# Optimization experiments

Hardware: AMD Instinct MI355X
Metric: run time of the kernel (lower is better)

## Reference

```python
import jax, jax.numpy as jnp
import numpy as np

TOP_K = 2
NUM_EXPERTS = 8

def setup_inputs() -> dict:
    key = jax.random.key(0)
    k_x, k_r, k_g, k_u, k_d = jax.random.split(key, 5)
    B, L, D, H, E = 1, 2048, 1024, 2048, NUM_EXPERTS
    scale = 0.02  # keep router logits / activations in a sane range
    return {
        "x": jax.random.normal(k_x, (B, L, D), dtype=jnp.float32),
        "router_w": jax.random.normal(k_r, (D, E), dtype=jnp.float32) * scale,
        "gate_w": jax.random.normal(k_g, (E, D, H), dtype=jnp.float32) * scale,
        "up_w": jax.random.normal(k_u, (E, D, H), dtype=jnp.float32) * scale,
        "down_w": jax.random.normal(k_d, (E, H, D), dtype=jnp.float32) * scale,
    }

def reference(x, router_w, gate_w, up_w, down_w):
    # x: (B, L, D)
    B, L, D = x.shape
    T = B * L
    E = router_w.shape[1]
    xf = x.reshape(T, D)

    # --- router: top-k softmax over selected logits (Mixtral-style) ---
    logits = xf @ router_w                      # (T, E)
    top_vals, top_idx = jax.lax.top_k(logits, TOP_K)  # (T, K)
    top_w = jax.nn.softmax(top_vals, axis=-1)   # (T, K)

    # combine weights scattered to dense (T, E); zeros for unrouted experts
    combine = jnp.zeros((T, E), dtype=x.dtype).at[
        jnp.arange(T)[:, None], top_idx
    ].add(top_w)

    # --- experts: SwiGLU, computed per expert, zero-weight tokens masked by combine ---
    gate = jnp.einsum('td,edh->eth', xf, gate_w)   # (E, T, H)
    up = jnp.einsum('td,edh->eth', xf, up_w)       # (E, T, H)
    hidden = jax.nn.silu(gate) * up                # (E, T, H)
    expert_out = jnp.einsum('eth,ehd->etd', hidden, down_w)  # (E, T, D)

    # --- weighted combine (equivalent to scatter_add over sorted assignments) ---
    y = jnp.einsum('etd,te->td', expert_out, combine)  # (T, D)
    return y.reshape(B, L, D)
```

## Files before the change

### kernel.cpp

```cpp
#include <hip/hip_runtime.h>
#include <hip/hip_bf16.h>
#include <stdint.h>

#define T_TOK 2048
#define DIM   1024
#define HDIM  2048
#define NE    8
#define ROWS_PAD 4224
#define TSLOTS 40

typedef __attribute__((ext_vector_type(8))) short bf16x8;
typedef __attribute__((ext_vector_type(4))) float f32x4;

__device__ __forceinline__ unsigned short f2bf(float f) {
    union { float f; unsigned int u; } v; v.f = f;
    unsigned int r = v.u + 0x7FFF + ((v.u >> 16) & 1);
    return (unsigned short)(r >> 16);
}

__device__ __forceinline__ void gload16(const void* g, void* l) {
    __builtin_amdgcn_global_load_lds(
        (const __attribute__((address_space(1))) void*)g,
        (__attribute__((address_space(3))) void*)l, 16, 0, 0);
}

__global__ void transpose_cvt(const float* __restrict__ in, unsigned short* __restrict__ out,
                              int R, int C) {
    __shared__ float tile[32][33];
    int b = blockIdx.z;
    int bx = blockIdx.x, by = blockIdx.y;
    int tx = threadIdx.x & 31, ty = threadIdx.x >> 5;
    const float* ip = in + (size_t)b * R * C;
    unsigned short* op = out + (size_t)b * R * C;
#pragma unroll
    for (int i = 0; i < 4; ++i) {
        int r = by * 32 + ty + i * 8;
        tile[ty + i * 8][tx] = ip[(size_t)r * C + bx * 32 + tx];
    }
    __syncthreads();
#pragma unroll
    for (int i = 0; i < 2; ++i) {
        int oc = i * 16 + (threadIdx.x >> 4);
        int orw2 = (threadIdx.x & 15) * 2;
        ushort2 v;
        v.x = f2bf(tile[orw2][oc]);
        v.y = f2bf(tile[orw2 + 1][oc]);
        *(ushort2*)&op[(size_t)(bx * 32 + oc) * R + by * 32 + orw2] = v;
    }
}

__global__ void router_kernel(const float* __restrict__ x, const float* __restrict__ rw,
                              int* __restrict__ counts, int* __restrict__ top_idx,
                              float* __restrict__ top_w) {
    int wid = (blockIdx.x * blockDim.x + threadIdx.x) >> 6;
    int lane = threadIdx.x & 63;
    if (wid >= T_TOK) return;
    float acc[NE];
#pragma unroll
    for (int e = 0; e < NE; ++e) acc[e] = 0.f;
    const float* xr = x + (size_t)wid * DIM;
    for (int i = lane; i < DIM; i += 64) {
        float xv = xr[i];
        const float* wr = rw + (size_t)i * NE;
#pragma unroll
        for (int e = 0; e < NE; ++e) acc[e] += xv * wr[e];
    }
#pragma unroll
    for (int off = 32; off; off >>= 1) {
#pragma unroll
        for (int e = 0; e < NE; ++e) acc[e] += __shfl_xor(acc[e], off, 64);
    }
    if (lane == 0) {
        float v0 = -1e30f, v1 = -1e30f; int i0 = 0, i1 = 0;
#pragma unroll
        for (int e = 0; e < NE; ++e) {
            float v = acc[e];
            if (v > v0) { v1 = v0; i1 = i0; v0 = v; i0 = e; }
            else if (v > v1) { v1 = v; i1 = e; }
        }
        float e1 = __expf(v1 - v0);
        float s = 1.f + e1;
        top_idx[wid * 2]     = i0;
        top_idx[wid * 2 + 1] = i1;
        top_w[wid * 2]     = 1.f / s;
        top_w[wid * 2 + 1] = e1 / s;
        atomicAdd(&counts[i0], 1);
        atomicAdd(&counts[i1], 1);
    }
}

__global__ void scan_kernel(const int* __restrict__ counts, int* __restrict__ offsets,
                            int* __restrict__ cursors,
                            int* __restrict__ tl_e, int* __restrict__ tl_m) {
    if (threadIdx.x == 0) {
        int run = 0;
        for (int e = 0; e < NE; ++e) { offsets[e] = run; cursors[e] = run; run += counts[e]; }
        int n = 0;
        for (int e = 0; e < NE; ++e) {
            int mt = (counts[e] + 127) >> 7;
            for (int m = 0; m < mt && n < 64; ++m) { tl_e[n] = e; tl_m[n] = m; ++n; }
        }
        for (; n < 64; ++n) tl_e[n] = -1;
    }
}

__global__ void gather_kernel(const float* __restrict__ x, const int* __restrict__ top_idx,
                              const float* __restrict__ top_w, int* __restrict__ cursors,
                              int* __restrict__ row_tok, float* __restrict__ row_w,
                              unsigned short* __restrict__ Abuf) {
    int t = blockIdx.x;
    __shared__ int pos[2];
    if (threadIdx.x < 2) {
        int k = threadIdx.x;
        int e = top_idx[t * 2 + k];
        int p = atomicAdd(&cursors[e], 1);
        pos[k] = p;
        row_tok[p] = t;
        row_w[p] = top_w[t * 2 + k];
    }
    __syncthreads();
    const float4* xr = (const float4*)(x + (size_t)t * DIM);
    float4 v = xr[threadIdx.x];
    ushort4 b;
    b.x = f2bf(v.x); b.y = f2bf(v.y); b.z = f2bf(v.z); b.w = f2bf(v.w);
    ushort4* A4 = (ushort4*)Abuf;
    A4[(size_t)pos[0] * (DIM / 4) + threadIdx.x] = b;
    A4[(size_t)pos[1] * (DIM / 4) + threadIdx.x] = b;
}

__global__ __launch_bounds__(256, 2)
void gemm1_kernel(const unsigned short* __restrict__ Abuf,
                  const unsigned short* __restrict__ WgT,
                  const unsigned short* __restrict__ WuT,
                  unsigned short* __restrict__ Hbuf,
                  const int* __restrict__ offsets, const int* __restrict__ counts,
                  const int* __restrict__ tl_e, const int* __restrict__ tl_m) {
    const int slot = blockIdx.y;
    const int e = tl_e[slot];
    if (e < 0) return;
    const int mtile = tl_m[slot];
    const int cnt = counts[e];
    const int n0 = blockIdx.x * 128;
    const int row0 = offsets[e] + mtile * 128;

    __shared__ unsigned short As[2][128 * 32];
    __shared__ unsigned short Bg[2][128 * 32];
    __shared__ unsigned short Bu[2][128 * 32];

    const int tid = threadIdx.x;
    const int lane = tid & 63;
    const int wave = tid >> 6;
    const int wm = wave >> 1, wn = wave & 1;

    f32x4 accg[4][4], accu[4][4];
#pragma unroll
    for (int i = 0; i < 4; ++i)
#pragma unroll
        for (int j = 0; j < 4; ++j) {
            accg[i][j] = (f32x4){0.f, 0.f, 0.f, 0.f};
            accu[i][j] = (f32x4){0.f, 0.f, 0.f, 0.f};
        }

    const int srow0 = tid >> 2;
    const int sc0 = tid & 3;
    const unsigned short* Aab = Abuf + (size_t)row0 * DIM;
    const unsigned short* Bgb = WgT + (size_t)e * HDIM * DIM + (size_t)n0 * DIM;
    const unsigned short* Bub = WuT + (size_t)e * HDIM * DIM + (size_t)n0 * DIM;

    auto stage = [&](int buf, int kt) {
#pragma unroll
        for (int i = 0; i < 2; ++i) {
            int row = i * 64 + srow0;
            int csrc = sc0 ^ ((row >> 1) & 3);
            size_t go = (size_t)row * DIM + kt + csrc * 8;
            int lo = (i * 256 + tid) * 8;
            gload16(Aab + go, &As[buf][lo]);
            gload16(Bgb + go, &Bg[buf][lo]);
            gload16(Bub + go, &Bu[buf][lo]);
        }
    };

    const int rsel = lane & 15;
    const int csrcf = lane >> 4;

    stage(0, 0);
    int cur = 0;
    for (int kt = 0; kt < DIM; kt += 32) {
        __syncthreads();
        if (kt + 32 < DIM) stage(cur ^ 1, kt + 32);
        const unsigned short* Ac = As[cur];
        const unsigned short* Bgc = Bg[cur];
        const unsigned short* Buc = Bu[cur];
        bf16x8 af[4], bg[4], bu[4];
#pragma unroll
        for (int i = 0; i < 4; ++i) {
            int ra = wm * 64 + i * 16 + rsel;
            af[i] = *(const bf16x8*)&Ac[ra * 32 + (csrcf ^ ((ra >> 1) & 3)) * 8];
            int rb = wn * 64 + i * 16 + rsel;
            int cb = (csrcf ^ ((rb >> 1) & 3)) * 8;
            bg[i] = *(const bf16x8*)&Bgc[rb * 32 + cb];
            bu[i] = *(const bf16x8*)&Buc[rb * 32 + cb];
        }
#pragma unroll
        for (int i = 0; i < 4; ++i)
#pragma unroll
            for (int j = 0; j < 4; ++j) {
                accg[i][j] = __builtin_amdgcn_mfma_f32_16x16x32_bf16(af[i], bg[j], accg[i][j], 0, 0, 0);
                accu[i][j] = __builtin_amdgcn_mfma_f32_16x16x32_bf16(af[i], bu[j], accu[i][j], 0, 0, 0);
            }
        cur ^= 1;
    }

    const int c = lane & 15, rbase = (lane >> 4) * 4;
    const int obase = offsets[e];
#pragma unroll
    for (int i = 0; i < 4; ++i) {
#pragma unroll
        for (int r = 0; r < 4; ++r) {
            int lrow = mtile * 128 + wm * 64 + i * 16 + rbase + r;
            if (lrow < cnt) {
                size_t orow = (size_t)(obase + lrow);
#pragma unroll
                for (int j = 0; j < 4; ++j) {
                    float g = accg[i][j][r], u = accu[i][j][r];
                    float h = g * u / (1.f + __expf(-g));
                    Hbuf[orow * HDIM + n0 + wn * 64 + j * 16 + c] = f2bf(h);
                }
            }
        }
    }
}

__global__ __launch_bounds__(256, 3)
void gemm2_kernel(const unsigned short* __restrict__ Hbuf,
                  const unsigned short* __restrict__ WdT,
                  float* __restrict__ y,
                  const int* __restrict__ offsets, const int* __restrict__ counts,
                  const int* __restrict__ row_tok, const float* __restrict__ row_w,
                  const int* __restrict__ tl_e, const int* __restrict__ tl_m) {
    const int slot = blockIdx.y;
    const int e = tl_e[slot];
    if (e < 0) return;
    const int mtile = tl_m[slot];
    const int kc = blockIdx.z;
    const int cnt = counts[e];
    const int n0 = blockIdx.x * 128;
    const int row0 = offsets[e] + mtile * 128;

    __shared__ unsigned short As[3][128 * 32];
    __shared__ unsigned short Bs[3][128 * 32];

    const int tid = threadIdx.x;
    const int lane = tid & 63;
    const int wave = tid >> 6;
    const int wm = wave >> 1, wn = wave & 1;

    f32x4 acc[4][4];
#pragma unroll
    for (int i = 0; i < 4; ++i)
#pragma unroll
        for (int j = 0; j < 4; ++j) acc[i][j] = (f32x4){0.f, 0.f, 0.f, 0.f};

    const int srow0 = tid >> 2;
    const int sc0 = tid & 3;
    const unsigned short* Aab = Hbuf + (size_t)row0 * HDIM;
    const unsigned short* Bbb = WdT + (size_t)e * DIM * HDIM + (size_t)n0 * HDIM;

    auto stage = [&](int buf, int kt) {
#pragma unroll
        for (int i = 0; i < 2; ++i) {
            int row = i * 64 + srow0;
            int csrc = sc0 ^ ((row >> 1) & 3);
            size_t go = (size_t)row * HDIM + kt + csrc * 8;
            int lo = (i * 256 + tid) * 8;
            gload16(Aab + go, &As[buf][lo]);
            gload16(Bbb + go, &Bs[buf][lo]);
        }
    };

    const int rsel = lane & 15;
    const int csrcf = lane >> 4;

    const int kbeg = kc * (HDIM / 2);
    const int NS = (HDIM / 2) / 32;

    stage(0, kbeg);
    stage(1, kbeg + 32);
    int cur = 0;
    for (int s = 0; s < NS; ++s) {
        if (s + 1 < NS) { asm volatile("s_waitcnt vmcnt(4)" ::: "memory"); }
        else            { asm volatile("s_waitcnt vmcnt(0)" ::: "memory"); }
        __builtin_amdgcn_s_barrier();
        if (s + 2 < NS) {
            int pb = cur + 2; if (pb >= 3) pb -= 3;
            stage(pb, kbeg + (s + 2) * 32);
        }
        const unsigned short* Ac = As[cur];
        const unsigned short* Bc = Bs[cur];
        bf16x8 af[4], bf[4];
#pragma unroll
        for (int i = 0; i < 4; ++i) {
            int ra = wm * 64 + i * 16 + rsel;
            af[i] = *(const bf16x8*)&Ac[ra * 32 + (csrcf ^ ((ra >> 1) & 3)) * 8];
            int rb = wn * 64 + i * 16 + rsel;
            bf[i] = *(const bf16x8*)&Bc[rb * 32 + (csrcf ^ ((rb >> 1) & 3)) * 8];
        }
#pragma unroll
        for (int i = 0; i < 4; ++i)
#pragma unroll
            for (int j = 0; j < 4; ++j)
                acc[i][j] = __builtin_amdgcn_mfma_f32_16x16x32_bf16(af[i], bf[j], acc[i][j], 0, 0, 0);
        ++cur; if (cur == 3) cur = 0;
    }

    const int c = lane & 15, rbase = (lane >> 4) * 4;
    const int obase = offsets[e];
#pragma unroll
    for (int i = 0; i < 4; ++i) {
#pragma unroll
        for (int r = 0; r < 4; ++r) {
            int lrow = mtile * 128 + wm * 64 + i * 16 + rbase + r;
            if (lrow < cnt) {
                int grow = obase + lrow;
                int tok = row_tok[grow];
                float w = row_w[grow];
#pragma unroll
                for (int j = 0; j < 4; ++j) {
                    atomicAdd(&y[(size_t)tok * DIM + n0 + wn * 64 + j * 16 + c], w * acc[i][j][r]);
                }
            }
        }
    }
}

extern "C" void kernel_launch(void* const* d_in, const int* in_sizes, int n_in,
                              void* d_out, int out_size, void* d_ws, size_t ws_size,
                              hipStream_t stream) {
    const float* x  = (const float*)d_in[0];
    const float* rw = (const float*)d_in[1];
    const float* gw = (const float*)d_in[2];
    const float* uw = (const float*)d_in[3];
    const float* dw = (const float*)d_in[4];
    float* y = (float*)d_out;

    char* ws = (char*)d_ws;
    int*   counts  = (int*)(ws + 0);
    int*   cursors = (int*)(ws + 32);
    int*   offsets = (int*)(ws + 64);
    int*   top_idx = (int*)(ws + 128);
    float* top_w   = (float*)(ws + 128 + 16384);
    int*   row_tok = (int*)(ws + 128 + 32768);
    float* row_w   = (float*)(ws + 128 + 32768 + 16896);
    int*   tl_e    = (int*)(ws + 128 + 32768 + 2 * 16896);
    int*   tl_m    = (int*)(ws + 128 + 32768 + 2 * 16896 + 256);
    size_t off = 128 + 32768 + 2 * 16896 + 512;
    off = (off + 255) & ~(size_t)255;
    unsigned short* Abuf = (unsigned short*)(ws + off); off += (size_t)ROWS_PAD * DIM * 2;
    unsigned short* Hbuf = (unsigned short*)(ws + off); off += (size_t)ROWS_PAD * HDIM * 2;
    unsigned short* WgT  = (unsigned short*)(ws + off); off += (size_t)NE * DIM * HDIM * 2;
    unsigned short* WuT  = (unsigned short*)(ws + off); off += (size_t)NE * DIM * HDIM * 2;
    unsigned short* WdT  = (unsigned short*)(ws + off); off += (size_t)NE * DIM * HDIM * 2;
    if (ws_size < off) return;

    hipMemsetAsync(counts, 0, 32, stream);
    hipMemsetAsync(d_out, 0, (size_t)out_size * 4, stream);

    transpose_cvt<<<dim3(HDIM / 32, DIM / 32, NE), 256, 0, stream>>>(gw, WgT, DIM, HDIM);
    transpose_cvt<<<dim3(HDIM / 32, DIM / 32, NE), 256, 0, stream>>>(uw, WuT, DIM, HDIM);
    transpose_cvt<<<dim3(DIM / 32, HDIM / 32, NE), 256, 0, stream>>>(dw, WdT, HDIM, DIM);

    router_kernel<<<T_TOK / 4, 256, 0, stream>>>(x, rw, counts, top_idx, top_w);
    scan_kernel<<<1, 64, 0, stream>>>(counts, offsets, cursors, tl_e, tl_m);
    gather_kernel<<<T_TOK, 256, 0, stream>>>(x, top_idx, top_w, cursors, row_tok, row_w, Abuf);

    gemm1_kernel<<<dim3(HDIM / 128, TSLOTS), 256, 0, stream>>>(Abuf, WgT, WuT, Hbuf,
                                                               offsets, counts, tl_e, tl_m);
    gemm2_kernel<<<dim3(DIM / 128, TSLOTS, 2), 256, 0, stream>>>(Hbuf, WdT, y, offsets, counts,
                                                                 row_tok, row_w, tl_e, tl_m);
}
```

Measured before the change: 278.8 us.

## Split gate/up across waves in gemm1 with narrower N tile and LDS exchange

The gemm1 tile shrinks from 128 to 64 columns, and the waves now specialize: half accumulate the gate projection and half the up projection. This halves accumulator registers so occupancy can go from 2 to 4 blocks per CU. The up results pass through LDS (rounded to bf16) to the gate waves, which apply SiLU and write H. In exchange the A tile is loaded twice as often per output, two extra barriers are added, and the up value loses some precision.

```diff
diff --git a/kernel.cpp b/kernel.cpp
--- a/kernel.cpp
+++ b/kernel.cpp
@@ -16,6 +16,11 @@
     union { float f; unsigned int u; } v; v.f = f;
     unsigned int r = v.u + 0x7FFF + ((v.u >> 16) & 1);
     return (unsigned short)(r >> 16);
+}
+
+__device__ __forceinline__ float bf2f(unsigned short b) {
+    union { unsigned int u; float f; } v; v.u = ((unsigned int)b) << 16;
+    return v.f;
 }
 
 __device__ __forceinline__ void gload16(const void* g, void* l) {
@@ -128,7 +133,7 @@
     A4[(size_t)pos[1] * (DIM / 4) + threadIdx.x] = b;
 }
 
-__global__ __launch_bounds__(256, 2)
+__global__ __launch_bounds__(256, 4)
 void gemm1_kernel(const unsigned short* __restrict__ Abuf,
                   const unsigned short* __restrict__ WgT,
                   const unsigned short* __restrict__ WuT,
@@ -140,28 +145,28 @@
     if (e < 0) return;
     const int mtile = tl_m[slot];
     const int cnt = counts[e];
-    const int n0 = blockIdx.x * 128;
+    const int n0 = blockIdx.x * 64;
     const int row0 = offsets[e] + mtile * 128;
 
-    __shared__ unsigned short As[2][128 * 32];
-    __shared__ unsigned short Bg[2][128 * 32];
-    __shared__ unsigned short Bu[2][128 * 32];
+    __shared__ __align__(16) unsigned char lds_raw[32768];
+    unsigned short* AsB = (unsigned short*)lds_raw;
+    unsigned short* BgB = (unsigned short*)(lds_raw + 16384);
+    unsigned short* BuB = (unsigned short*)(lds_raw + 24576);
+    unsigned short* ex  = (unsigned short*)lds_raw;
 
     const int tid = threadIdx.x;
     const int lane = tid & 63;
     const int wave = tid >> 6;
-    const int wm = wave >> 1, wn = wave & 1;
-
-    f32x4 accg[4][4], accu[4][4];
+    const int wm = wave >> 1;
+    const int wu = wave & 1;
+
+    f32x4 acc[4][4];
 #pragma unroll
     for (int i = 0; i < 4; ++i)
 #pragma unroll
-        for (int j = 0; j < 4; ++j) {
-            accg[i][j] = (f32x4){0.f, 0.f, 0.f, 0.f};
-            accu[i][j] = (f32x4){0.f, 0.f, 0.f, 0.f};
-        }
-
-    const int srow0 = tid >> 2;
+        for (int j = 0; j < 4; ++j) acc[i][j] = (f32x4){0.f, 0.f, 0.f, 0.f};
+
+    const int srow = tid >> 2;
     const int sc0 = tid & 3;
     const unsigned short* Aab = Abuf + (size_t)row0 * DIM;
     const unsigned short* Bgb = WgT + (size_t)e * HDIM * DIM + (size_t)n0 * DIM;
@@ -170,14 +175,14 @@
     auto stage = [&](int buf, int kt) {
 #pragma unroll
         for (int i = 0; i < 2; ++i) {
-            int row = i * 64 + srow0;
+            int row = i * 64 + srow;
             int csrc = sc0 ^ ((row >> 1) & 3);
-            size_t go = (size_t)row * DIM + kt + csrc * 8;
-            int lo = (i * 256 + tid) * 8;
-            gload16(Aab + go, &As[buf][lo]);
-            gload16(Bgb + go, &Bg[buf][lo]);
-            gload16(Bub + go, &Bu[buf][lo]);
-        }
+            gload16(Aab + (size_t)row * DIM + kt + csrc * 8,
+                    AsB + buf * 4096 + (i * 256 + tid) * 8);
+        }
+        int csrcb = sc0 ^ ((srow >> 1) & 3);
+        gload16(Bgb + (size_t)srow * DIM + kt + csrcb * 8, BgB + buf * 2048 + tid * 8);
+        gload16(Bub + (size_t)srow * DIM + kt + csrcb * 8, BuB + buf * 2048 + tid * 8);
     };
 
     const int rsel = lane & 15;
@@ -188,43 +193,55 @@
     for (int kt = 0; kt < DIM; kt += 32) {
         __syncthreads();
         if (kt + 32 < DIM) stage(cur ^ 1, kt + 32);
-        const unsigned short* Ac = As[cur];
-        const unsigned short* Bgc = Bg[cur];
-        const unsigned short* Buc = Bu[cur];
-        bf16x8 af[4], bg[4], bu[4];
+        const unsigned short* Ac = AsB + cur * 4096;
+        const unsigned short* Bc = (wu ? BuB : BgB) + cur * 2048;
+        bf16x8 af[4], bb[4];
 #pragma unroll
         for (int i = 0; i < 4; ++i) {
             int ra = wm * 64 + i * 16 + rsel;
             af[i] = *(const bf16x8*)&Ac[ra * 32 + (csrcf ^ ((ra >> 1) & 3)) * 8];
-            int rb = wn * 64 + i * 16 + rsel;
-            int cb = (csrcf ^ ((rb >> 1) & 3)) * 8;
-            bg[i] = *(const bf16x8*)&Bgc[rb * 32 + cb];
-            bu[i] = *(const bf16x8*)&Buc[rb * 32 + cb];
+            int rb = i * 16 + rsel;
+            bb[i] = *(const bf16x8*)&Bc[rb * 32 + (csrcf ^ ((rb >> 1) & 3)) * 8];
         }
 #pragma unroll
         for (int i = 0; i < 4; ++i)
 #pragma unroll
-            for (int j = 0; j < 4; ++j) {
-                accg[i][j] = __builtin_amdgcn_mfma_f32_16x16x32_bf16(af[i], bg[j], accg[i][j], 0, 0, 0);
-                accu[i][j] = __builtin_amdgcn_mfma_f32_16x16x32_bf16(af[i], bu[j], accu[i][j], 0, 0, 0);
-            }
+            for (int j = 0; j < 4; ++j)
+                acc[i][j] = __builtin_amdgcn_mfma_f32_16x16x32_bf16(af[i], bb[j], acc[i][j], 0, 0, 0);
         cur ^= 1;
     }
 
     const int c = lane & 15, rbase = (lane >> 4) * 4;
     const int obase = offsets[e];
-#pragma unroll
-    for (int i = 0; i < 4; ++i) {
-#pragma unroll
-        for (int r = 0; r < 4; ++r) {
-            int lrow = mtile * 128 + wm * 64 + i * 16 + rbase + r;
-            if (lrow < cnt) {
-                size_t orow = (size_t)(obase + lrow);
-#pragma unroll
-                for (int j = 0; j < 4; ++j) {
-                    float g = accg[i][j][r], u = accu[i][j][r];
-                    float h = g * u / (1.f + __expf(-g));
-                    Hbuf[orow * HDIM + n0 + wn * 64 + j * 16 + c] = f2bf(h);
+    __syncthreads();
+    if (wu) {
+#pragma unroll
+        for (int i = 0; i < 4; ++i)
+#pragma unroll
+            for (int r = 0; r < 4; ++r) {
+                int row64 = i * 16 + rbase + r;
+#pragma unroll
+                for (int j = 0; j < 4; ++j)
+                    ex[wm * 4096 + row64 * 64 + j * 16 + c] = f2bf(acc[i][j][r]);
+            }
+    }
+    __syncthreads();
+    if (!wu) {
+#pragma unroll
+        for (int i = 0; i < 4; ++i) {
+#pragma unroll
+            for (int r = 0; r < 4; ++r) {
+                int row64 = i * 16 + rbase + r;
+                int lrow = mtile * 128 + wm * 64 + row64;
+                if (lrow < cnt) {
+                    size_t orow = (size_t)(obase + lrow);
+#pragma unroll
+                    for (int j = 0; j < 4; ++j) {
+                        float g = acc[i][j][r];
+                        float u = bf2f(ex[wm * 4096 + row64 * 64 + j * 16 + c]);
+                        float h = g * u / (1.f + __expf(-g));
+                        Hbuf[orow * HDIM + n0 + j * 16 + c] = f2bf(h);
+                    }
                 }
             }
         }
@@ -373,8 +390,8 @@
     scan_kernel<<<1, 64, 0, stream>>>(counts, offsets, cursors, tl_e, tl_m);
     gather_kernel<<<T_TOK, 256, 0, stream>>>(x, top_idx, top_w, cursors, row_tok, row_w, Abuf);
 
-    gemm1_kernel<<<dim3(HDIM / 128, TSLOTS), 256, 0, stream>>>(Abuf, WgT, WuT, Hbuf,
-                                                               offsets, counts, tl_e, tl_m);
+    gemm1_kernel<<<dim3(HDIM / 64, TSLOTS), 256, 0, stream>>>(Abuf, WgT, WuT, Hbuf,
+                                                              offsets, counts, tl_e, tl_m);
     gemm2_kernel<<<dim3(DIM / 128, TSLOTS, 2), 256, 0, stream>>>(Hbuf, WdT, y, offsets, counts,
                                                                  row_tok, row_w, tl_e, tl_m);
 }
```

New measurement: 269.6 us. -3.3%, faster.
